# Kernel tuning notes

Measured on AMD Instinct MI355X. Metric: run time of the kernel, lower is better.

Reference implementation:

```python
import jax, jax.numpy as jnp
import numpy as np

N, L, S = 512, 1024, 32   # batch, latent dim, spatial (S*S == L)
F = 32 * S * S            # flattened encoder conv features (last conv = 32 ch)
H = 512                   # hidden width of latent MLP heads


def _lrelu(x):
    return jnp.where(x >= 0, x, 0.01 * x)


def _bn(x):
    # BatchNorm2d in training mode, gamma=1, beta=0 (default init)
    m = x.mean((0, 2, 3), keepdims=True)
    v = x.var((0, 2, 3), keepdims=True)
    return (x - m) * jax.lax.rsqrt(v + 1e-5)


def _conv(x, w, b):
    y = jax.lax.conv_general_dilated(x, w, (1, 1), 'SAME',
                                     dimension_numbers=('NCHW', 'OIHW', 'NCHW'))
    return y + b[None, :, None, None]


def _block(x, w, b):
    return _lrelu(_bn(_conv(x, w, b)))


def setup_inputs() -> dict:
    key = jax.random.key(0)
    ks = jax.random.split(key, 16)
    r = lambda k, s, sc: jax.random.normal(k, s, jnp.float32) * sc
    return {
        'x': r(ks[0], (N, 1, S, S), 1.0),
        'eps_c': r(ks[1], (N, L), 1.0),
        'eps_s': r(ks[2], (N, L), 1.0),
        'enc_cw1': r(ks[3], (2, 32, 1, 3, 3), 0.1),   'enc_cb1': jnp.zeros((2, 32)),
        'enc_cw2': r(ks[4], (2, 64, 32, 3, 3), 0.05), 'enc_cb2': jnp.zeros((2, 64)),
        'enc_cw3': r(ks[5], (2, 32, 64, 3, 3), 0.05), 'enc_cb3': jnp.zeros((2, 32)),
        'enc_muW1': r(ks[6], (2, H, F), 0.005), 'enc_muB1': jnp.zeros((2, H)),
        'enc_muW2': r(ks[7], (2, L, H), 0.02),  'enc_muB2': jnp.zeros((2, L)),
        'enc_vaW1': r(ks[8], (2, H, F), 0.005), 'enc_vaB1': jnp.zeros((2, H)),
        'enc_vaW2': r(ks[9], (2, L, H), 0.02),  'enc_vaB2': jnp.zeros((2, L)),
        'dec_cw1': r(ks[10], (2, 32, 1, 3, 3), 0.1),   'dec_cb1': jnp.zeros((2, 32)),
        'dec_cw2': r(ks[11], (2, 64, 32, 3, 3), 0.05), 'dec_cb2': jnp.zeros((2, 64)),
        'dec_cw3': r(ks[12], (2, 1, 64, 3, 3), 0.05),  'dec_cb3': jnp.zeros((2, 1)),
    }


def reference(x, eps_c, eps_s,
              enc_cw1, enc_cb1, enc_cw2, enc_cb2, enc_cw3, enc_cb3,
              enc_muW1, enc_muB1, enc_muW2, enc_muB2,
              enc_vaW1, enc_vaB1, enc_vaW2, enc_vaB2,
              dec_cw1, dec_cb1, dec_cw2, dec_cb2, dec_cw3, dec_cb3):
    def encode(i):
        h = _block(x, enc_cw1[i], enc_cb1[i])
        h = _block(h, enc_cw2[i], enc_cb2[i])
        h = _block(h, enc_cw3[i], enc_cb3[i])
        f = h.reshape(N, -1)                                   # [N, F]
        mu = _lrelu(_lrelu(f @ enc_muW1[i].T + enc_muB1[i]) @ enc_muW2[i].T + enc_muB2[i])
        lv = _lrelu(_lrelu(f @ enc_vaW1[i].T + enc_vaB1[i]) @ enc_vaW2[i].T + enc_vaB2[i])
        return mu, lv                                          # each [N, L]

    def decode(z, i):
        h = z.reshape(N, 1, S, S)
        h = _block(h, dec_cw1[i], dec_cb1[i])
        h = _block(h, dec_cw2[i], dec_cb2[i])
        h = _block(h, dec_cw3[i], dec_cb3[i])
        return h.reshape(N, 1, S, S)

    class_mu, class_logvar = encode(0)
    style_mu, style_logvar = encode(1)

    # precision-weighted product-of-experts group evidence (vectorized)
    precision = jnp.exp(-style_logvar)                  # 1/var, [N, L]
    group_var = 1.0 / precision.sum(0)                  # [L]
    group_mu = (style_mu * precision).sum(0) * group_var  # [L]
    group_logvar = jnp.log(group_var)

    # reparameterize
    z_c = eps_c * jnp.exp(0.5 * class_logvar) + class_mu          # [N, L]
    z_s = eps_s * jnp.exp(0.5 * group_logvar)[None] + group_mu[None]  # [N, L]

    output_c = decode(z_c, 0)
    output_s = jax.nn.relu(decode(z_s, 1))
    output = output_c * output_s                        # [N, 1, S, S]

    kl1 = -0.5 * jnp.sum(1.0 + class_logvar) + 0.5 * (
        jnp.sum(class_mu ** 2) + jnp.sum(jnp.exp(class_logvar) ** 2))
    kl2 = -0.5 * jnp.sum(1.0 + group_logvar) + 0.5 * (
        jnp.sum(group_mu ** 2) + jnp.sum(jnp.exp(group_logvar) ** 2))
    recon = (jnp.exp(x) - jnp.exp(output)) ** 2
    loss = -kl1 + kl2 + recon                           # [N, 1, S, S]
    return loss, output
```

## Files before the change

kernel.cpp:

```cpp
#include <hip/hip_runtime.h>

constexpr int N_   = 512;
constexpr int PIX  = 1024;
constexpr int L_   = 1024;
constexpr int F_   = 32768;
constexpr int H_   = 512;
constexpr float IC_ = 1.0f / (float)(512 * 1024);

__device__ __forceinline__ float lrelu(float t) { return t >= 0.f ? t : 0.01f * t; }

using frag  = __attribute__((ext_vector_type(8))) short;
using f32x4 = __attribute__((ext_vector_type(4))) float;
using s4    = __attribute__((ext_vector_type(4))) short;

__device__ __forceinline__ void split_bf16(float v, short& hi, short& lo) {
    const unsigned b = __float_as_uint(v);
    hi = (short)(b >> 16);
    const float hf = __uint_as_float(b & 0xFFFF0000u);
    lo = (short)(__float_as_uint(v - hf) >> 16);
}

__device__ __forceinline__ frag ld2(const short* p) {
    union { frag f; struct { unsigned long long a, b; } u; } x;
    x.u.a = *(const unsigned long long*)(p);
    x.u.b = *(const unsigned long long*)(p + 4);
    return x.f;
}

__global__ __launch_bounds__(256) void wsplit6_kernel(
    const float* __restrict__ w0, const float* __restrict__ w1,
    const float* __restrict__ w2, const float* __restrict__ w3,
    const float* __restrict__ w4, const float* __restrict__ w5,
    short* __restrict__ hi, short* __restrict__ lo)
{
    const int layer = blockIdx.y;
    const float* W = layer == 0 ? w0 : layer == 1 ? w1 : layer == 2 ? w2 :
                     layer == 3 ? w3 : layer == 4 ? w4 : w5;
    const int CIN  = (layer == 1 || layer == 3) ? 64 : 32;
    const int NCOT = (layer == 1 || layer == 3) ? 2 : 4;
    const int idx = blockIdx.x * 256 + threadIdx.x;
    const int j    = idx & 7;
    const int lane = (idx >> 3) & 63;
    const int q    = lane >> 4, lm = lane & 15;
    const int blk  = idx >> 9;
    const int cot  = blk % NCOT;
    const int rest = blk / NCOT;
    const int pos  = rest % 9;
    const int cc   = rest / 9;
    const int co = cot * 16 + lm;
    const int ci = cc * 32 + q * 8 + j;
    short h, l;
    split_bf16(W[((size_t)co * CIN + ci) * 9 + pos], h, l);
    hi[layer * 18432 + idx] = h;
    lo[layer * 18432 + idx] = l;
}

template<int CIN, int COUT, bool BN_IN>
__global__ __launch_bounds__(256) void conv_mfma(
    const float* __restrict__ in, const short* __restrict__ wh,
    const short* __restrict__ wl, const float* __restrict__ bias,
    float* __restrict__ out, const float* __restrict__ stats_in,
    float* __restrict__ stats_out)
{
    constexpr int NCOT = COUT / 16;
    constexpr int NCH  = CIN / 32;
    constexpr int STR  = 36;
    constexpr int PLsh = 340 * STR;
    __shared__ __align__(16) short hiL[PLsh];
    __shared__ __align__(16) short loL[PLsh];
    __shared__ float red[2 * COUT];
    __shared__ float bnm[64], bni[64];
    const int tid  = threadIdx.x;
    const int n    = blockIdx.x >> 2;
    const int y0   = (blockIdx.x & 3) << 3;
    const int lane = tid & 63;
    const int wv   = tid >> 6;
    const int lm   = lane & 15;
    const int q    = lane >> 4;

    if (tid < 2 * COUT) red[tid] = 0.f;
    if (BN_IN && tid < CIN) {
        const float m  = stats_in[tid] * IC_;
        const float qq = stats_in[CIN + tid] * IC_;
        bnm[tid] = m;
        bni[tid] = rsqrtf(qq - m * m + 1e-5f);
    }
    __syncthreads();

    f32x4 acc[NCOT][4];
#pragma unroll
    for (int t = 0; t < NCOT; ++t)
#pragma unroll
        for (int pt = 0; pt < 4; ++pt) acc[t][pt] = {0.f, 0.f, 0.f, 0.f};

    const int rs0 = tid / 34, cs0 = tid % 34;
    const int idx1 = tid + 256;
    const int rs1 = idx1 / 34, cs1 = idx1 % 34;
    const int gr0 = y0 - 1 + rs0, gc0 = cs0 - 1;
    const int gr1 = y0 - 1 + rs1, gc1 = cs1 - 1;
    const bool in1 = idx1 < 340;
    const bool ok0 = ((unsigned)gr0 < 32u) && ((unsigned)gc0 < 32u);
    const bool ok1 = in1 && ((unsigned)gr1 < 32u) && ((unsigned)gc1 < 32u);
    const int  po0 = gr0 * 32 + gc0;
    const int  po1 = gr1 * 32 + gc1;

    const float* inb = in + ((size_t)n * CIN << 10);

    frag ahA[NCOT], alA[NCOT], ahB[NCOT], alB[NCOT];

    auto LDW = [&](frag (&dh)[NCOT], frag (&dl)[NCOT], int posAbs) {
#pragma unroll
        for (int t = 0; t < NCOT; ++t) {
            const size_t wb = (size_t)((posAbs * NCOT + t) * 512 + lane * 8);
            dh[t] = *(const frag*)&wh[wb];
            dl[t] = *(const frag*)&wl[wb];
        }
    };

    auto COMPUTE = [&](int pos, frag (&fh)[NCOT], frag (&fl)[NCOT]) {
        const int ky = pos / 3, kx = pos - ky * 3;
        __builtin_amdgcn_s_setprio(1);
#pragma unroll
        for (int pt = 0; pt < 4; ++pt) {
            const int ptile = wv * 4 + pt;
            const int row = ptile >> 1;
            const int col = ((ptile & 1) << 4) + lm;
            const int loff = ((row + ky) * 34 + col + kx) * STR + q * 8;
            const frag bh = ld2(&hiL[loff]);
            const frag bl = ld2(&loL[loff]);
#pragma unroll
            for (int t = 0; t < NCOT; ++t) {
                acc[t][pt] = __builtin_amdgcn_mfma_f32_16x16x32_bf16(
                    fh[t], bh, acc[t][pt], 0, 0, 0);
                acc[t][pt] = __builtin_amdgcn_mfma_f32_16x16x32_bf16(
                    fh[t], bl, acc[t][pt], 0, 0, 0);
                acc[t][pt] = __builtin_amdgcn_mfma_f32_16x16x32_bf16(
                    fl[t], bh, acc[t][pt], 0, 0, 0);
            }
        }
        __builtin_amdgcn_s_setprio(0);
    };

#pragma unroll 1
    for (int cc = 0; cc < NCH; ++cc) {
        if (cc) __syncthreads();

        LDW(ahA, alA, cc * 9 + 0);

#pragma unroll 1
        for (int cb = 0; cb < 32; cb += 16) {
            float v0r[16], v1r[16];
#pragma unroll
            for (int u = 0; u < 16; ++u) {
                const int cg = cc * 32 + cb + u;
                v0r[u] = ok0 ? inb[((size_t)cg << 10) + po0] : 0.f;
                v1r[u] = ok1 ? inb[((size_t)cg << 10) + po1] : 0.f;
            }
#pragma unroll
            for (int u4 = 0; u4 < 16; u4 += 4) {
                s4 h0v, l0v, h1v, l1v;
#pragma unroll
                for (int e = 0; e < 4; ++e) {
                    const int ci = cb + u4 + e;
                    const int cg = cc * 32 + ci;
                    float v0 = v0r[u4 + e];
                    if (BN_IN && ok0) v0 = lrelu((v0 - bnm[cg]) * bni[cg]);
                    short h, l;
                    split_bf16(v0, h, l);
                    h0v[e] = h; l0v[e] = l;
                    float v1 = v1r[u4 + e];
                    if (BN_IN && ok1) v1 = lrelu((v1 - bnm[cg]) * bni[cg]);
                    short h1, l1;
                    split_bf16(v1, h1, l1);
                    h1v[e] = h1; l1v[e] = l1;
                }
                *(s4*)&hiL[tid * STR + cb + u4] = h0v;
                *(s4*)&loL[tid * STR + cb + u4] = l0v;
                if (in1) {
                    *(s4*)&hiL[idx1 * STR + cb + u4] = h1v;
                    *(s4*)&loL[idx1 * STR + cb + u4] = l1v;
                }
            }
        }
        __syncthreads();

#pragma unroll 1
        for (int pos = 0; pos < 8; pos += 2) {
            LDW(ahB, alB, cc * 9 + pos + 1);
            COMPUTE(pos, ahA, alA);
            LDW(ahA, alA, cc * 9 + pos + 2);
            COMPUTE(pos + 1, ahB, alB);
        }
        COMPUTE(8, ahA, alA);
    }

    float* ob = out + ((size_t)n * COUT << 10);
#pragma unroll
    for (int t = 0; t < NCOT; ++t) {
#pragma unroll
        for (int r = 0; r < 4; ++r) {
            const int co = t * 16 + q * 4 + r;
            const float b = bias[co];
            float s = 0.f, sq = 0.f;
#pragma unroll
            for (int pt = 0; pt < 4; ++pt) {
                const float v = acc[t][pt][r] + b;
                ob[((size_t)co << 10) + (y0 << 5) + ((wv * 4 + pt) << 4) + lm] = v;
                s += v; sq += v * v;
            }
#pragma unroll
            for (int off = 8; off > 0; off >>= 1) {
                s  += __shfl_down(s, off, 64);
                sq += __shfl_down(sq, off, 64);
            }
            if (lm == 0) {
                atomicAdd(&red[co], s);
                atomicAdd(&red[COUT + co], sq);
            }
        }
    }
    __syncthreads();
    if (tid < 2 * COUT) atomicAdd(&stats_out[tid], red[tid]);
}

template<int CIN, int COPB, bool BN_IN>
__global__ __launch_bounds__(256) void conv3x3(
    const float* __restrict__ in, const float* __restrict__ w,
    const float* __restrict__ bias, float* __restrict__ out,
    const float* __restrict__ stats_in, float* __restrict__ stats_out,
    int Cout)
{
    constexpr int CT = (CIN < 4) ? CIN : 4;
    __shared__ float tile[CT * PIX];
    __shared__ float red[2 * COPB];
    const int groups = Cout / COPB;
    const int n   = blockIdx.x / groups;
    const int co0 = (blockIdx.x % groups) * COPB;
    const int tid = threadIdx.x;
    const int x   = tid & 31;
    const int y0  = (tid >> 5) * 4;

    float acc[COPB][4];
#pragma unroll
    for (int c = 0; c < COPB; ++c)
#pragma unroll
        for (int j = 0; j < 4; ++j) acc[c][j] = 0.f;

    const float* inbase = in + (size_t)n * CIN * PIX;

#pragma unroll 1
    for (int s0 = 0; s0 < CIN; s0 += CT) {
        __syncthreads();
#pragma unroll
        for (int s = 0; s < CT; ++s) {
            float4 v = ((const float4*)(inbase + (size_t)(s0 + s) * PIX))[tid];
            if (BN_IN) {
                const int c = s0 + s;
                const float m   = stats_in[c] * IC_;
                const float q   = stats_in[CIN + c] * IC_;
                const float inv = rsqrtf(q - m * m + 1e-5f);
                v.x = lrelu((v.x - m) * inv);
                v.y = lrelu((v.y - m) * inv);
                v.z = lrelu((v.z - m) * inv);
                v.w = lrelu((v.w - m) * inv);
            }
            ((float4*)tile)[s * 256 + tid] = v;
        }
        __syncthreads();
#pragma unroll 2
        for (int s = 0; s < CT; ++s) {
            const int ci = s0 + s;
            const float* tp = tile + s * PIX;
            float r[6][3];
#pragma unroll
            for (int ry = 0; ry < 6; ++ry) {
                const int yy = y0 + ry - 1;
                const bool yok = (unsigned)yy < 32u;
#pragma unroll
                for (int cx = 0; cx < 3; ++cx) {
                    const int xx = x + cx - 1;
                    const bool ok = yok && ((unsigned)xx < 32u);
                    r[ry][cx] = ok ? tp[yy * 32 + xx] : 0.f;
                }
            }
#pragma unroll
            for (int c = 0; c < COPB; ++c) {
                const float* wp = w + ((size_t)(co0 + c) * CIN + ci) * 9;
#pragma unroll
                for (int ky = 0; ky < 3; ++ky)
#pragma unroll
                    for (int kx = 0; kx < 3; ++kx) {
                        const float wv = wp[ky * 3 + kx];
#pragma unroll
                        for (int j = 0; j < 4; ++j)
                            acc[c][j] += r[ky + j][kx] * wv;
                    }
            }
        }
    }

    if (tid < 2 * COPB) red[tid] = 0.f;
    __syncthreads();
#pragma unroll
    for (int c = 0; c < COPB; ++c) {
        const float b = bias[co0 + c];
        float* ob = out + (((size_t)n * Cout + co0 + c) << 10);
        float s = 0.f, q = 0.f;
#pragma unroll
        for (int j = 0; j < 4; ++j) {
            const float v = acc[c][j] + b;
            ob[(y0 + j) * 32 + x] = v;
            s += v; q += v * v;
        }
#pragma unroll
        for (int off = 32; off > 0; off >>= 1) {
            s += __shfl_down(s, off, 64);
            q += __shfl_down(q, off, 64);
        }
        if ((tid & 63) == 0) {
            atomicAdd(&red[c], s);
            atomicAdd(&red[COPB + c], q);
        }
    }
    __syncthreads();
    if (tid < COPB)
        atomicAdd(&stats_out[co0 + tid], red[tid]);
    else if (tid < 2 * COPB)
        atomicAdd(&stats_out[Cout + co0 + tid - COPB], red[tid]);
}

template<bool BN_A>
__global__ __launch_bounds__(256) void gemm_mfma(
    const float* __restrict__ A0, const float* __restrict__ A1,
    const float* __restrict__ B0, const float* __restrict__ B1,
    float* __restrict__ C0, float* __restrict__ C1,
    int K, int Nh, int kchunk, int xph,
    const float* __restrict__ bnstats, int Cin)
{
    __shared__ short AhL[4096], AlL[4096], BhL[4096], BlL[4096];
    const int tid  = threadIdx.x;
    const int head = blockIdx.x / xph;
    const int n0   = (blockIdx.x % xph) * 128;
    const int m0   = blockIdx.y * 128;
    const float* A = head ? A1 : A0;
    const float* B = head ? B1 : B0;
    float*       C = head ? C1 : C0;
    const int k0 = blockIdx.z * kchunk;
    const int k1 = k0 + kchunk;

    const int lane = tid & 63;
    const int wv   = tid >> 6;
    const int wm   = wv & 1;
    const int wn   = wv >> 1;
    const int lm   = lane & 15;
    const int q    = lane >> 4;

    const int srow = tid >> 1;
    const int smt  = srow >> 4;
    const int slm  = srow & 15;
    const int sq0  = (tid & 1) * 2;
    const int ks   = (tid & 1) * 16;

    f32x4 acc[4][4];
#pragma unroll
    for (int i = 0; i < 4; ++i)
#pragma unroll
        for (int j = 0; j < 4; ++j) acc[i][j] = {0.f, 0.f, 0.f, 0.f};

    auto cv8 = [](float4 u, float4 w2, frag& h, frag& l) {
        const float v[8] = {u.x, u.y, u.z, u.w, w2.x, w2.y, w2.z, w2.w};
#pragma unroll
        for (int e = 0; e < 8; ++e) {
            short hh, ll;
            split_bf16(v[e], hh, ll);
            h[e] = hh; l[e] = ll;
        }
    };

    float4 a4[4], b4[4];
    auto LOADAB = [&](int kb) {
        const float* Ap = A + (size_t)(m0 + srow) * K + kb + ks;
        const float* Bp = B + (size_t)(n0 + srow) * K + kb + ks;
#pragma unroll
        for (int g = 0; g < 4; ++g) a4[g] = ((const float4*)Ap)[g];
#pragma unroll
        for (int g = 0; g < 4; ++g) b4[g] = ((const float4*)Bp)[g];
    };

    LOADAB(k0);

#pragma unroll 1
    for (int kb = k0; kb < k1; kb += 32) {
        if (BN_A) {
            const int c = (kb + ks) >> 10;
            const float m   = bnstats[c] * IC_;
            const float qq  = bnstats[Cin + c] * IC_;
            const float inv = rsqrtf(qq - m * m + 1e-5f);
#pragma unroll
            for (int g = 0; g < 4; ++g) {
                a4[g].x = lrelu((a4[g].x - m) * inv);
                a4[g].y = lrelu((a4[g].y - m) * inv);
                a4[g].z = lrelu((a4[g].z - m) * inv);
                a4[g].w = lrelu((a4[g].w - m) * inv);
            }
        }

        frag ah0, al0, ah1, al1, bh0, bl0, bh1, bl1;
        cv8(a4[0], a4[1], ah0, al0);
        cv8(a4[2], a4[3], ah1, al1);
        cv8(b4[0], b4[1], bh0, bl0);
        cv8(b4[2], b4[3], bh1, bl1);

        __syncthreads();
        const int o0 = ((smt * 4 + sq0) * 16 + slm) * 8;
        const int o1 = ((smt * 4 + sq0 + 1) * 16 + slm) * 8;
        *(frag*)&AhL[o0] = ah0;  *(frag*)&AhL[o1] = ah1;
        *(frag*)&AlL[o0] = al0;  *(frag*)&AlL[o1] = al1;
        *(frag*)&BhL[o0] = bh0;  *(frag*)&BhL[o1] = bh1;
        *(frag*)&BlL[o0] = bl0;  *(frag*)&BlL[o1] = bl1;
        __syncthreads();

        frag fah[4], fal[4], fbh[4], fbl[4];
#pragma unroll
        for (int t = 0; t < 4; ++t) {
            const int oa = (((wm * 4 + t) * 4 + q) * 16 + lm) * 8;
            const int ob = (((wn * 4 + t) * 4 + q) * 16 + lm) * 8;
            fah[t] = *(const frag*)&AhL[oa];
            fal[t] = *(const frag*)&AlL[oa];
            fbh[t] = *(const frag*)&BhL[ob];
            fbl[t] = *(const frag*)&BlL[ob];
        }

        if (kb + 32 < k1) LOADAB(kb + 32);
#pragma unroll
        for (int i = 0; i < 4; ++i)
#pragma unroll
            for (int j = 0; j < 4; ++j) {
                acc[i][j] = __builtin_amdgcn_mfma_f32_16x16x32_bf16(
                    fah[i], fbh[j], acc[i][j], 0, 0, 0);
                acc[i][j] = __builtin_amdgcn_mfma_f32_16x16x32_bf16(
                    fah[i], fbl[j], acc[i][j], 0, 0, 0);
                acc[i][j] = __builtin_amdgcn_mfma_f32_16x16x32_bf16(
                    fal[i], fbh[j], acc[i][j], 0, 0, 0);
            }
    }

#pragma unroll
    for (int i = 0; i < 4; ++i) {
        const int m = m0 + wm * 64 + i * 16 + q * 4;
#pragma unroll
        for (int j = 0; j < 4; ++j) {
            const int n = n0 + wn * 64 + j * 16 + lm;
            float* cp = C + (size_t)m * Nh + n;
#pragma unroll
            for (int r = 0; r < 4; ++r)
                atomicAdd(cp + (size_t)r * Nh, acc[i][j][r]);
        }
    }
}

__global__ __launch_bounds__(256) void bias_lrelu2_kernel(
    float* __restrict__ bufa, const float* __restrict__ ba,
    float* __restrict__ bufb, const float* __restrict__ bb,
    int Nn, int per)
{
    const int idx = blockIdx.x * 256 + threadIdx.x;
    if (idx < per) {
        bufa[idx] = lrelu(bufa[idx] + ba[idx % Nn]);
    } else {
        const int j = idx - per;
        bufb[j] = lrelu(bufb[j] + bb[j % Nn]);
    }
}

__device__ __forceinline__ void block_reduce_atomic(float t, float* target)
{
#pragma unroll
    for (int off = 32; off > 0; off >>= 1) t += __shfl_down(t, off, 64);
    __shared__ float lt[4];
    const int wave = threadIdx.x >> 6, lane = threadIdx.x & 63;
    if (lane == 0) lt[wave] = t;
    __syncthreads();
    if (threadIdx.x == 0) atomicAdd(target, lt[0] + lt[1] + lt[2] + lt[3]);
}

__global__ __launch_bounds__(256) void poe_kernel(
    const float* __restrict__ mu1, const float* __restrict__ lv1,
    float* __restrict__ gmu, float* __restrict__ glv, float* __restrict__ kl)
{
    const int l = blockIdx.x * 256 + threadIdx.x;
    float sp = 0.f, sm = 0.f;
    for (int n = 0; n < N_; ++n) {
        const float lv = lv1[(size_t)n * L_ + l];
        const float p  = expf(-lv);
        sp += p;
        sm += mu1[(size_t)n * L_ + l] * p;
    }
    const float gv = 1.f / sp;
    const float gm = sm * gv;
    const float gl = -logf(sp);
    gmu[l] = gm;
    glv[l] = gl;
    const float t = -0.5f * (1.f + gl) + 0.5f * (gm * gm + gv * gv);
    block_reduce_atomic(t, &kl[1]);
}

__global__ __launch_bounds__(256) void reparam_kernel(
    const float* __restrict__ mu0, const float* __restrict__ lv0,
    const float* __restrict__ eps_c, const float* __restrict__ eps_s,
    const float* __restrict__ gmu, const float* __restrict__ glv,
    float* __restrict__ zc, float* __restrict__ zs, float* __restrict__ kl)
{
    const int idx = blockIdx.x * 256 + threadIdx.x;
    const int l = idx & (L_ - 1);
    const float m  = mu0[idx];
    const float lv = lv0[idx];
    zc[idx] = eps_c[idx] * expf(0.5f * lv) + m;
    zs[idx] = eps_s[idx] * expf(0.5f * glv[l]) + gmu[l];
    const float e = expf(lv);
    const float t = -0.5f * (1.f + lv) + 0.5f * (m * m + e * e);
    block_reduce_atomic(t, &kl[0]);
}

__global__ __launch_bounds__(256) void final_kernel(
    const float* __restrict__ x, const float* __restrict__ oc,
    const float* __restrict__ os, const float* __restrict__ stC,
    const float* __restrict__ stS, const float* __restrict__ kl,
    float* __restrict__ out)
{
    const int idx = blockIdx.x * 256 + threadIdx.x;
    const float mc = stC[0] * IC_, qc = stC[1] * IC_;
    const float ivc = rsqrtf(qc - mc * mc + 1e-5f);
    const float ms = stS[0] * IC_, qs = stS[1] * IC_;
    const float ivs = rsqrtf(qs - ms * ms + 1e-5f);
    const float tc = lrelu((oc[idx] - mc) * ivc);
    const float ts = fmaxf((os[idx] - ms) * ivs, 0.f);
    const float o = tc * ts;
    const float d = expf(x[idx]) - expf(o);
    out[idx]            = -kl[0] + kl[1] + d * d;
    out[N_ * PIX + idx] = o;
}

extern "C" void kernel_launch(void* const* d_in, const int* in_sizes, int n_in,
                              void* d_out, int out_size, void* d_ws, size_t ws_size,
                              hipStream_t stream)
{
    const float* x        = (const float*)d_in[0];
    const float* eps_c    = (const float*)d_in[1];
    const float* eps_s    = (const float*)d_in[2];
    const float* enc_cw1  = (const float*)d_in[3];
    const float* enc_cb1  = (const float*)d_in[4];
    const float* enc_cw2  = (const float*)d_in[5];
    const float* enc_cb2  = (const float*)d_in[6];
    const float* enc_cw3  = (const float*)d_in[7];
    const float* enc_cb3  = (const float*)d_in[8];
    const float* enc_muW1 = (const float*)d_in[9];
    const float* enc_muB1 = (const float*)d_in[10];
    const float* enc_muW2 = (const float*)d_in[11];
    const float* enc_muB2 = (const float*)d_in[12];
    const float* enc_vaW1 = (const float*)d_in[13];
    const float* enc_vaB1 = (const float*)d_in[14];
    const float* enc_vaW2 = (const float*)d_in[15];
    const float* enc_vaB2 = (const float*)d_in[16];
    const float* dec_cw1  = (const float*)d_in[17];
    const float* dec_cb1  = (const float*)d_in[18];
    const float* dec_cw2  = (const float*)d_in[19];
    const float* dec_cb2  = (const float*)d_in[20];
    const float* dec_cw3  = (const float*)d_in[21];
    const float* dec_cb3  = (const float*)d_in[22];
    float* out = (float*)d_out;

    float* ws   = (float*)d_ws;
    float* bufA = ws;
    float* bufB = bufA + (size_t)N_ * 64 * PIX;
    float* h1   = bufB + (size_t)N_ * 32 * PIX;
    float* h2   = h1 + N_ * H_;
    float* mu0  = h2 + N_ * H_;
    float* lv0  = mu0 + N_ * L_;
    float* mu1  = lv0 + N_ * L_;
    float* lv1  = mu1 + N_ * L_;
    float* zc   = lv1 + N_ * L_;
    float* zs   = zc + N_ * L_;
    float* oc   = zs + N_ * L_;
    float* os   = oc + N_ * L_;
    float* gmu  = os + N_ * L_;
    float* glv  = gmu + L_;
    float* stats = glv + L_;
    float* kl   = stats + 12 * 128;
    short* wsh  = (short*)(kl + 4);
    short* wsl  = wsh + 6 * 18432;

    auto st  = [&](int s) { return stats + 128 * s; };
    auto whp = [&](int layer) { return wsh + layer * 18432; };
    auto wlp = [&](int layer) { return wsl + layer * 18432; };

    hipMemsetAsync(stats, 0, (12 * 128 + 4) * sizeof(float), stream);

    wsplit6_kernel<<<dim3(72, 6), 256, 0, stream>>>(
        enc_cw2, enc_cw3, enc_cw2 + 64 * 32 * 9, enc_cw3 + 32 * 64 * 9,
        dec_cw2, dec_cw2 + 64 * 32 * 9, wsh, wsl);

    for (int i = 0; i < 2; ++i) {
        const float* cw1 = enc_cw1 + (size_t)i * 32 * 9;
        const float* cb1 = enc_cb1 + (size_t)i * 32;
        const float* cb2 = enc_cb2 + (size_t)i * 64;
        const float* cb3 = enc_cb3 + (size_t)i * 32;

        conv3x3<1, 16, false><<<N_ * 2, 256, 0, stream>>>(
            x, cw1, cb1, bufB, nullptr, st(i * 3 + 0), 32);
        conv_mfma<32, 64, true><<<N_ * 4, 256, 0, stream>>>(
            bufB, whp(i * 2), wlp(i * 2), cb2, bufA, st(i * 3 + 0), st(i * 3 + 1));
        conv_mfma<64, 32, true><<<N_ * 4, 256, 0, stream>>>(
            bufA, whp(i * 2 + 1), wlp(i * 2 + 1), cb3, bufB, st(i * 3 + 1), st(i * 3 + 2));

        const float* W1m = enc_muW1 + (size_t)i * H_ * F_;
        const float* B1m = enc_muB1 + (size_t)i * H_;
        const float* W2m = enc_muW2 + (size_t)i * L_ * H_;
        const float* B2m = enc_muB2 + (size_t)i * L_;
        const float* W1v = enc_vaW1 + (size_t)i * H_ * F_;
        const float* B1v = enc_vaB1 + (size_t)i * H_;
        const float* W2v = enc_vaW2 + (size_t)i * L_ * H_;
        const float* B2v = enc_vaB2 + (size_t)i * L_;
        float* mu_i = (i == 0) ? mu0 : mu1;
        float* lv_i = (i == 0) ? lv0 : lv1;

        hipMemsetAsync(h1, 0, (size_t)2 * N_ * H_ * sizeof(float), stream);
        gemm_mfma<true><<<dim3(8, 4, 16), 256, 0, stream>>>(
            bufB, bufB, W1m, W1v, h1, h2, F_, H_, 2048, 4, st(i * 3 + 2), 32);
        bias_lrelu2_kernel<<<(2 * N_ * H_) / 256, 256, 0, stream>>>(
            h1, B1m, h2, B1v, H_, N_ * H_);

        hipMemsetAsync(mu_i, 0, (size_t)2 * N_ * L_ * sizeof(float), stream);
        gemm_mfma<false><<<dim3(16, 4, 4), 256, 0, stream>>>(
            h1, h2, W2m, W2v, mu_i, lv_i, H_, L_, 128, 8, nullptr, 0);
        bias_lrelu2_kernel<<<(2 * N_ * L_) / 256, 256, 0, stream>>>(
            mu_i, B2m, lv_i, B2v, L_, N_ * L_);
    }

    poe_kernel<<<L_ / 256, 256, 0, stream>>>(mu1, lv1, gmu, glv, kl);
    reparam_kernel<<<(N_ * L_) / 256, 256, 0, stream>>>(
        mu0, lv0, eps_c, eps_s, gmu, glv, zc, zs, kl);

    for (int i = 0; i < 2; ++i) {
        const float* cw1 = dec_cw1 + (size_t)i * 32 * 9;
        const float* cb1 = dec_cb1 + (size_t)i * 32;
        const float* cb2 = dec_cb2 + (size_t)i * 64;
        const float* cw3 = dec_cw3 + (size_t)i * 64 * 9;
        const float* cb3 = dec_cb3 + (size_t)i * 1;
        const float* zi = (i == 0) ? zc : zs;
        float* oi = (i == 0) ? oc : os;

        conv3x3<1, 16, false><<<N_ * 2, 256, 0, stream>>>(
            zi, cw1, cb1, bufB, nullptr, st(6 + i * 3 + 0), 32);
        conv_mfma<32, 64, true><<<N_ * 4, 256, 0, stream>>>(
            bufB, whp(4 + i), wlp(4 + i), cb2, bufA, st(6 + i * 3 + 0), st(6 + i * 3 + 1));
        conv3x3<64, 1, true><<<N_, 256, 0, stream>>>(
            bufA, cw3, cb3, oi, st(6 + i * 3 + 1), st(6 + i * 3 + 2), 1);
    }

    final_kernel<<<(N_ * PIX) / 256, 256, 0, stream>>>(
        x, oc, os, st(8), st(11), kl, out);
}
```

Baseline: 1.466 ms.

## Double split-K for encoder GEMMs, hoist BN stats, widen conv staging

Split-K for both encoder MLP GEMMs goes from 16 to 32 and from 4 to 8 chunks. That doubles the grid to fill more CUs, at the cost of more atomic accumulation traffic into the output. BN mean and inverse std for the first GEMM are now computed once per block instead of every k-step. This relies on each 1024-wide k-chunk lying within a single channel. The conv input staging now loads all 32 channels in one unrolled pass instead of two passes of 16, which raises register pressure.

```diff
diff --git a/kernel.cpp b/kernel.cpp
--- a/kernel.cpp
+++ b/kernel.cpp
@@ -147,38 +147,37 @@
 
         LDW(ahA, alA, cc * 9 + 0);
 
-#pragma unroll 1
-        for (int cb = 0; cb < 32; cb += 16) {
-            float v0r[16], v1r[16];
-#pragma unroll
-            for (int u = 0; u < 16; ++u) {
-                const int cg = cc * 32 + cb + u;
+        {
+            float v0r[32], v1r[32];
+#pragma unroll
+            for (int u = 0; u < 32; ++u) {
+                const int cg = cc * 32 + u;
                 v0r[u] = ok0 ? inb[((size_t)cg << 10) + po0] : 0.f;
                 v1r[u] = ok1 ? inb[((size_t)cg << 10) + po1] : 0.f;
             }
 #pragma unroll
-            for (int u4 = 0; u4 < 16; u4 += 4) {
+            for (int u4 = 0; u4 < 32; u4 += 4) {
                 s4 h0v, l0v, h1v, l1v;
 #pragma unroll
                 for (int e = 0; e < 4; ++e) {
-                    const int ci = cb + u4 + e;
+                    const int ci = u4 + e;
                     const int cg = cc * 32 + ci;
-                    float v0 = v0r[u4 + e];
+                    float v0 = v0r[ci];
                     if (BN_IN && ok0) v0 = lrelu((v0 - bnm[cg]) * bni[cg]);
                     short h, l;
                     split_bf16(v0, h, l);
                     h0v[e] = h; l0v[e] = l;
-                    float v1 = v1r[u4 + e];
+                    float v1 = v1r[ci];
                     if (BN_IN && ok1) v1 = lrelu((v1 - bnm[cg]) * bni[cg]);
                     short h1, l1;
                     split_bf16(v1, h1, l1);
                     h1v[e] = h1; l1v[e] = l1;
                 }
-                *(s4*)&hiL[tid * STR + cb + u4] = h0v;
-                *(s4*)&loL[tid * STR + cb + u4] = l0v;
+                *(s4*)&hiL[tid * STR + u4] = h0v;
+                *(s4*)&loL[tid * STR + u4] = l0v;
                 if (in1) {
-                    *(s4*)&hiL[idx1 * STR + cb + u4] = h1v;
-                    *(s4*)&loL[idx1 * STR + cb + u4] = l1v;
+                    *(s4*)&hiL[idx1 * STR + u4] = h1v;
+                    *(s4*)&loL[idx1 * STR + u4] = l1v;
                 }
             }
         }
@@ -361,6 +360,14 @@
     const int sq0  = (tid & 1) * 2;
     const int ks   = (tid & 1) * 16;
 
+    float bn_m = 0.f, bn_inv = 1.f;
+    if (BN_A) {
+        const int c = k0 >> 10;
+        bn_m = bnstats[c] * IC_;
+        const float qq = bnstats[Cin + c] * IC_;
+        bn_inv = rsqrtf(qq - bn_m * bn_m + 1e-5f);
+    }
+
     f32x4 acc[4][4];
 #pragma unroll
     for (int i = 0; i < 4; ++i)
@@ -392,16 +399,12 @@
 #pragma unroll 1
     for (int kb = k0; kb < k1; kb += 32) {
         if (BN_A) {
-            const int c = (kb + ks) >> 10;
-            const float m   = bnstats[c] * IC_;
-            const float qq  = bnstats[Cin + c] * IC_;
-            const float inv = rsqrtf(qq - m * m + 1e-5f);
 #pragma unroll
             for (int g = 0; g < 4; ++g) {
-                a4[g].x = lrelu((a4[g].x - m) * inv);
-                a4[g].y = lrelu((a4[g].y - m) * inv);
-                a4[g].z = lrelu((a4[g].z - m) * inv);
-                a4[g].w = lrelu((a4[g].w - m) * inv);
+                a4[g].x = lrelu((a4[g].x - bn_m) * bn_inv);
+                a4[g].y = lrelu((a4[g].y - bn_m) * bn_inv);
+                a4[g].z = lrelu((a4[g].z - bn_m) * bn_inv);
+                a4[g].w = lrelu((a4[g].w - bn_m) * bn_inv);
             }
         }
 
@@ -432,6 +435,7 @@
         }
 
         if (kb + 32 < k1) LOADAB(kb + 32);
+
 #pragma unroll
         for (int i = 0; i < 4; ++i)
 #pragma unroll
@@ -625,14 +629,14 @@
         float* lv_i = (i == 0) ? lv0 : lv1;
 
         hipMemsetAsync(h1, 0, (size_t)2 * N_ * H_ * sizeof(float), stream);
-        gemm_mfma<true><<<dim3(8, 4, 16), 256, 0, stream>>>(
-            bufB, bufB, W1m, W1v, h1, h2, F_, H_, 2048, 4, st(i * 3 + 2), 32);
+        gemm_mfma<true><<<dim3(8, 4, 32), 256, 0, stream>>>(
+            bufB, bufB, W1m, W1v, h1, h2, F_, H_, 1024, 4, st(i * 3 + 2), 32);
         bias_lrelu2_kernel<<<(2 * N_ * H_) / 256, 256, 0, stream>>>(
             h1, B1m, h2, B1v, H_, N_ * H_);
 
         hipMemsetAsync(mu_i, 0, (size_t)2 * N_ * L_ * sizeof(float), stream);
-        gemm_mfma<false><<<dim3(16, 4, 4), 256, 0, stream>>>(
-            h1, h2, W2m, W2v, mu_i, lv_i, H_, L_, 128, 8, nullptr, 0);
+        gemm_mfma<false><<<dim3(16, 4, 8), 256, 0, stream>>>(
+            h1, h2, W2m, W2v, mu_i, lv_i, H_, L_, 64, 8, nullptr, 0);
         bias_lrelu2_kernel<<<(2 * N_ * L_) / 256, 256, 0, stream>>>(
             mu_i, B2m, lv_i, B2v, L_, N_ * L_);
     }
```

New measurement: 1.527 ms. 1.04x slower.
